# Optimization experiments

Hardware: AMD Instinct MI355X
Metric: run time of the kernel (lower is better)

## Reference

```python
import jax, jax.numpy as jnp
import numpy as np

N = 20000        # nodes
E = 1000000      # typed message-passing edges
R_REL = 32       # num relation types (== out_dim)
H = 128          # hidden_dim
IN = 128         # in_dim
B = 8            # num bases
ET = 20000       # target edges for decoder


def setup_inputs() -> dict:
    key = jax.random.key(0)
    ks = jax.random.split(key, 14)
    s = 0.05  # small init scale to keep relu/sigmoid in a sane range
    x = jax.random.normal(ks[0], (N, IN), jnp.float32)
    edge_index = jax.random.randint(ks[1], (2, E), 0, N, dtype=jnp.int64)
    etype = jax.random.randint(ks[2], (E,), 0, R_REL)
    edge_attr = jax.nn.one_hot(etype, R_REL, dtype=jnp.float32)  # one-hot so nonzero() == (arange(E), etype)
    target_edge_index = jax.random.randint(ks[3], (2, ET), 0, N, dtype=jnp.int64)
    return {
        'x': x,
        'edge_index': edge_index,
        'edge_attr': edge_attr,
        'target_edge_index': target_edge_index,
        'bases1': jax.random.normal(ks[4], (B, IN, H), jnp.float32) * s,
        'comp1': jax.random.normal(ks[5], (R_REL, B), jnp.float32) * s,
        'root1': jax.random.normal(ks[6], (IN, H), jnp.float32) * s,
        'bias1': jnp.zeros((H,), jnp.float32),
        'bases2': jax.random.normal(ks[7], (B, H, H), jnp.float32) * s,
        'comp2': jax.random.normal(ks[8], (R_REL, B), jnp.float32) * s,
        'root2': jax.random.normal(ks[9], (H, H), jnp.float32) * s,
        'bias2': jnp.zeros((H,), jnp.float32),
        'R_mat': jax.random.normal(ks[10], (H, H), jnp.float32) * s,
        'D': jax.random.normal(ks[11], (R_REL, H), jnp.float32) * s,
    }


def _rgcn(x, src, dst, etype, bases, comp, root, bias):
    # PyG-style RGCNConv with basis decomposition and per-relation mean aggregation.
    x_src = x[src]                                   # [E, in]  (memory-bound gather)
    seg = dst * R_REL + etype                        # segment per (dst node, relation)
    summ = jax.ops.segment_sum(x_src, seg, num_segments=N * R_REL)          # [N*R, in]
    cnt = jax.ops.segment_sum(jnp.ones((src.shape[0],), x.dtype), seg,
                              num_segments=N * R_REL)
    m = (summ / jnp.maximum(cnt, 1.0)[:, None]).reshape(N, R_REL, -1)       # per-relation mean
    W = jnp.einsum('rb,bio->rio', comp, bases)       # [R, in, out] relation weights from bases
    return jnp.einsum('nri,rio->no', m, W) + x @ root + bias


def reference(x, edge_index, edge_attr, target_edge_index,
              bases1, comp1, root1, bias1,
              bases2, comp2, root2, bias2,
              R_mat, D):
    # torch.nonzero(one-hot edge_attr) -> edges == arange(E), edge_type == argmax
    etype = jnp.argmax(edge_attr, axis=1)
    src, dst = edge_index[0], edge_index[1]
    h = jax.nn.relu(_rgcn(x, src, dst, etype, bases1, comp1, root1, bias1))   # dropout = identity (eval)
    h = jax.nn.relu(_rgcn(h, src, dst, etype, bases2, comp2, root2, bias2))
    x1 = h[target_edge_index[0]]                     # [ET, H]
    x2 = h[target_edge_index[1]]                     # [ET, H]
    # DEDICOM decoder: diag(D_r) @ R @ diag(D_r); equivalent to the diag-of-matmul-chain in the source
    M = D[:, :, None] * R_mat[None, :, :] * D[:, None, :]   # [R, H, H]
    out = jnp.einsum('ei,rij,ej->er', x1, M, x2)             # [ET, R]
    return jax.nn.sigmoid(out)
```

## Files before the change

kernel.cpp:

```cpp
#include <hip/hip_runtime.h>
#include <hip/hip_bf16.h>
#include <math.h>

#define NND 20000
#define NE  1000000
#define RREL 32
#define HD 128
#define NB 8
#define NT 20000
#define KCAT 1152
#define NBLK 64
#define CHUNK ((NE + NBLK - 1) / NBLK)

typedef short bf16x8 __attribute__((ext_vector_type(8)));
typedef float f32x4 __attribute__((ext_vector_type(4)));

static __device__ __forceinline__ unsigned short f2bf(float f){
  union { float f; unsigned int u; } c; c.f = f;
  unsigned int r = c.u + 0x7FFF + ((c.u >> 16) & 1);
  return (unsigned short)(r >> 16);
}
static __device__ __forceinline__ float bf2f(unsigned short s){
  union { unsigned int u; float f; } c; c.u = ((unsigned int)s) << 16;
  return c.f;
}

__global__ __launch_bounds__(256) void k_etype(
    const float* __restrict__ ea, int* __restrict__ etype)
{
  int e = blockIdx.x*256 + threadIdx.x;
  if (e >= NE) return;
  const float4* row = (const float4*)(ea + (size_t)e*RREL);
  int bi = 0;
  #pragma unroll
  for (int q=0;q<8;q++){
    float4 v = row[q];
    if (v.x > 0.5f) bi = q*4;
    if (v.y > 0.5f) bi = q*4+1;
    if (v.z > 0.5f) bi = q*4+2;
    if (v.w > 0.5f) bi = q*4+3;
  }
  etype[e] = bi;
}

__global__ __launch_bounds__(1024) void k_hist(const int* __restrict__ ei,
                                               int* __restrict__ ghist)
{
  __shared__ int h[NND/2];
  int t = threadIdx.x, b = blockIdx.x;
  for (int i=t; i<NND/2; i+=1024) h[i] = 0;
  __syncthreads();
  int e0 = b*CHUNK, e1 = min(e0+CHUNK, NE);
  for (int e=e0+t; e<e1; e+=1024){
    int dst = ei[NE + e];
    atomicAdd(&h[dst>>1], 1 << ((dst&1)*16));
  }
  __syncthreads();
  for (int i=t; i<NND/2; i+=1024){
    int v = h[i];
    ghist[(size_t)(2*i  )*NBLK + b] = v & 0xFFFF;
    ghist[(size_t)(2*i+1)*NBLK + b] = (v >> 16) & 0xFFFF;
  }
}

__global__ __launch_bounds__(256) void k_rowsum(const int* __restrict__ ghist,
                                                int* __restrict__ node_cnt)
{
  int t = threadIdx.x;
  int n = blockIdx.x*4 + (t>>6);
  int lane = t & 63;
  int v = ghist[(size_t)n*NBLK + lane];
  #pragma unroll
  for (int d=32; d>0; d>>=1) v += __shfl_down(v, d);
  if (lane == 0) node_cnt[n] = v;
}

__global__ __launch_bounds__(1024) void k_scan(const int* __restrict__ node_cnt,
                                               int* __restrict__ node_off)
{
  __shared__ int part[1024];
  int t = threadIdx.x;
  const int CH = (NND + 1023)/1024;
  int base = t*CH;
  int s = 0;
  for (int i=0;i<CH;i++){ int idx = base+i; if (idx<NND) s += node_cnt[idx]; }
  part[t] = s;
  __syncthreads();
  for (int d=1; d<1024; d<<=1){
    int v = part[t];
    int u = (t>=d) ? part[t-d] : 0;
    __syncthreads();
    part[t] = v + u;
    __syncthreads();
  }
  int run = (t==0) ? 0 : part[t-1];
  for (int i=0;i<CH;i++){ int idx=base+i; if (idx<NND){ node_off[idx]=run; run += node_cnt[idx]; } }
  if (t==1023) node_off[NND] = part[1023];
}

__global__ __launch_bounds__(256) void k_scanB(int* __restrict__ ghist,
                                               const int* __restrict__ node_off)
{
  int t = threadIdx.x;
  int n = blockIdx.x*4 + (t>>6);
  int lane = t & 63;
  int v = ghist[(size_t)n*NBLK + lane];
  int x = v;
  #pragma unroll
  for (int d=1; d<64; d<<=1){ int y = __shfl_up(x, d); if (lane >= d) x += y; }
  ghist[(size_t)n*NBLK + lane] = node_off[n] + x - v;
}

__global__ __launch_bounds__(1024) void k_scatter2(
    const int* __restrict__ ei, const int* __restrict__ etype,
    const int* __restrict__ ghist, int2* __restrict__ sorted)
{
  __shared__ int h[NND/2];
  int t = threadIdx.x, b = blockIdx.x;
  for (int i=t; i<NND/2; i+=1024) h[i] = 0;
  __syncthreads();
  int e0 = b*CHUNK, e1 = min(e0+CHUNK, NE);
  for (int e=e0+t; e<e1; e+=1024){
    int dst = ei[NE + e];
    int sh = (dst&1)*16;
    int old = atomicAdd(&h[dst>>1], 1 << sh);
    int rank = (old >> sh) & 0xFFFF;
    int pos = ghist[(size_t)dst*NBLK + b] + rank;
    sorted[pos] = make_int2(ei[e], etype[e]);
  }
}

__global__ __launch_bounds__(256) void k_cnt(const int2* __restrict__ sorted,
                                             const int* __restrict__ node_off,
                                             float* __restrict__ inv)
{
  int t = threadIdx.x;
  int n = blockIdx.x*4 + (t>>6);
  int lane = t & 63;
  int r = lane & 31, half = lane >> 5;
  int p0 = node_off[n], p1 = node_off[n+1];
  int c = 0;
  for (int p=p0+half; p<p1; p+=2) c += (sorted[p].y == r);
  c += __shfl_down(c, 32);
  if (lane < 32) inv[(size_t)n*RREL + lane] = 1.0f / fmaxf((float)c, 1.0f);
}

__global__ __launch_bounds__(256) void k_castX(const float* __restrict__ x,
                                               unsigned short* __restrict__ xb)
{
  int i = blockIdx.x*256 + threadIdx.x;
  if (i >= NND*HD/8) return;
  const float4* p = (const float4*)(x + (size_t)i*8);
  float4 a = p[0], b = p[1];
  unsigned int o0 = f2bf(a.x) | ((unsigned int)f2bf(a.y)<<16);
  unsigned int o1 = f2bf(a.z) | ((unsigned int)f2bf(a.w)<<16);
  unsigned int o2 = f2bf(b.x) | ((unsigned int)f2bf(b.y)<<16);
  unsigned int o3 = f2bf(b.z) | ((unsigned int)f2bf(b.w)<<16);
  *(uint4*)(xb + (size_t)i*8) = make_uint4(o0,o1,o2,o3);
}

__global__ __launch_bounds__(64) void k_agg(
    const int2* __restrict__ sorted, const int* __restrict__ node_off,
    const float* __restrict__ inv_cnt, const float* __restrict__ comp,
    const unsigned short* __restrict__ xb, unsigned short* __restrict__ mbxb)
{
  int n = blockIdx.x;
  int lane = threadIdx.x;
  float a0[NB], a1[NB];
  #pragma unroll
  for (int b=0;b<NB;b++){ a0[b]=0.f; a1[b]=0.f; }
  int p0 = node_off[n], p1 = node_off[n+1];
  const float* icr = inv_cnt + (size_t)n*RREL;
  for (int p=p0; p<p1; ++p){
    int2 se = sorted[p];
    float x0 = bf2f(xb[(size_t)se.x*HD + lane]);
    float x1 = bf2f(xb[(size_t)se.x*HD + 64 + lane]);
    float ic = icr[se.y];
    const float* cr = comp + se.y*NB;
    #pragma unroll
    for (int b=0;b<NB;b++){
      float c = cr[b]*ic;
      a0[b] += c*x0;
      a1[b] += c*x1;
    }
  }
  unsigned short* o = mbxb + (size_t)n*KCAT;
  #pragma unroll
  for (int b=0;b<NB;b++){
    o[b*HD + lane]      = f2bf(a0[b]);
    o[b*HD + 64 + lane] = f2bf(a1[b]);
  }
  o[1024 + lane]      = xb[(size_t)n*HD + lane];
  o[1024 + 64 + lane] = xb[(size_t)n*HD + 64 + lane];
}

__global__ __launch_bounds__(256) void k_prepW(
    const float* __restrict__ bases, const float* __restrict__ root,
    unsigned short* __restrict__ Wt)
{
  int idx = blockIdx.x*256 + threadIdx.x;
  if (idx >= HD*(KCAT/8)) return;
  int o  = idx / (KCAT/8);
  int k0 = (idx % (KCAT/8))*8;
  unsigned short tmp[8];
  #pragma unroll
  for (int q=0;q<8;q++){
    int k = k0+q;
    float v = (k < 1024) ? bases[(size_t)k*HD + o] : root[(size_t)(k-1024)*HD + o];
    tmp[q] = f2bf(v);
  }
  *(uint4*)(Wt + (size_t)o*KCAT + k0) = *(uint4*)tmp;
}

__global__ __launch_bounds__(256) void k_gemm2(
    const unsigned short* __restrict__ A, const unsigned short* __restrict__ Wt,
    const float* __restrict__ bias, float* __restrict__ outF,
    unsigned short* __restrict__ outB)
{
  int t = threadIdx.x, bm = blockIdx.x;
  int lane = t & 63, w = t >> 6, g = lane >> 4, c = lane & 15;
  const unsigned short* arow = A + (size_t)(bm*16 + c)*KCAT;
  const unsigned short* wt0 = Wt + (size_t)((w*2+0)*16 + c)*KCAT;
  const unsigned short* wt1 = Wt + (size_t)((w*2+1)*16 + c)*KCAT;
  f32x4 acc0 = {0.f,0.f,0.f,0.f}, acc1 = {0.f,0.f,0.f,0.f};
  for (int kk=0; kk<KCAT/32; ++kk){
    int koff = kk*32 + 8*g;
    bf16x8 a  = *(const bf16x8*)(arow + koff);
    bf16x8 b0 = *(const bf16x8*)(wt0 + koff);
    bf16x8 b1 = *(const bf16x8*)(wt1 + koff);
    acc0 = __builtin_amdgcn_mfma_f32_16x16x32_bf16(a, b0, acc0, 0,0,0);
    acc1 = __builtin_amdgcn_mfma_f32_16x16x32_bf16(a, b1, acc1, 0,0,0);
  }
  int orow = bm*16 + 4*g;
  #pragma unroll
  for (int nt=0; nt<2; ++nt){
    int o = (w*2+nt)*16 + c;
    float bi = bias[o];
    f32x4 acc = nt ? acc1 : acc0;
    #pragma unroll
    for (int q=0; q<4; ++q){
      int rr = orow + q;
      float v = fmaxf(acc[q] + bi, 0.f);
      outF[(size_t)rr*HD + o] = v;
      outB[(size_t)rr*HD + o] = f2bf(v);
    }
  }
}

__global__ __launch_bounds__(256) void k_prep(const float* __restrict__ Rm,
                                              const float* __restrict__ D,
                                              unsigned short* __restrict__ Ms)
{
  int r = blockIdx.x, t = threadIdx.x;
  int i = blockIdx.y*16 + (t>>4);
  int j0 = (t&15)*8;
  float di = D[r*HD + i];
  float4 dj0 = *(const float4*)(D + r*HD + j0);
  float4 dj1 = *(const float4*)(D + r*HD + j0 + 4);
  float4 r0 = *(const float4*)(Rm + (size_t)i*HD + j0);
  float4 r1 = *(const float4*)(Rm + (size_t)i*HD + j0 + 4);
  unsigned int o0 = f2bf(di*dj0.x*r0.x) | ((unsigned int)f2bf(di*dj0.y*r0.y)<<16);
  unsigned int o1 = f2bf(di*dj0.z*r0.z) | ((unsigned int)f2bf(di*dj0.w*r0.w)<<16);
  unsigned int o2 = f2bf(di*dj1.x*r1.x) | ((unsigned int)f2bf(di*dj1.y*r1.y)<<16);
  unsigned int o3 = f2bf(di*dj1.z*r1.z) | ((unsigned int)f2bf(di*dj1.w*r1.w)<<16);
  *(uint4*)(Ms + (size_t)(r*HD + i)*HD + j0) = make_uint4(o0,o1,o2,o3);
}

__global__ __launch_bounds__(256) void k_dec3(
    const float* __restrict__ h2, const int* __restrict__ tgt,
    const unsigned short* __restrict__ Ms, float* __restrict__ out)
{
  __shared__ __align__(16) unsigned short vb[64*136];
  __shared__ __align__(16) float uf[64*132];
  __shared__ __align__(16) float red[64*8];
  int t = threadIdx.x;
  int bm = blockIdx.x;
  int lane = t & 63, w = t >> 6, g = lane >> 4, c = lane & 15;

  {
    int e = t >> 2, seg = t & 3;
    int eg = bm*64 + e;
    bool ok = (eg < NT);
    int n0 = ok ? tgt[eg] : 0;
    int n1 = ok ? tgt[NT + eg] : 0;
    const float4* pu = (const float4*)(h2 + (size_t)n0*HD + seg*32);
    const float4* pv = (const float4*)(h2 + (size_t)n1*HD + seg*32);
    float* ufr = uf + e*132 + seg*32;
    unsigned int* vbr = (unsigned int*)vb + e*68 + seg*16;
    #pragma unroll
    for (int q=0;q<8;q++){
      float4 u4 = ok ? pu[q] : make_float4(0,0,0,0);
      float4 v4 = ok ? pv[q] : make_float4(0,0,0,0);
      *(float4*)(ufr + q*4) = u4;
      vbr[q*2+0] = (unsigned int)f2bf(v4.x) | ((unsigned int)f2bf(v4.y)<<16);
      vbr[q*2+1] = (unsigned int)f2bf(v4.z) | ((unsigned int)f2bf(v4.w)<<16);
    }
  }
  __syncthreads();

  for (int r=0; r<RREL; ++r){
    f32x4 acc[2][4];
    #pragma unroll
    for (int mm=0;mm<2;mm++)
      #pragma unroll
      for (int nt=0;nt<4;nt++){ f32x4 z = {0.f,0.f,0.f,0.f}; acc[mm][nt] = z; }
    #pragma unroll
    for (int kk=0; kk<4; ++kk){
      int koff = kk*32 + 8*g;
      bf16x8 a0 = *(const bf16x8*)(Ms + (size_t)(r*HD + (2*w+0)*16 + c)*HD + koff);
      bf16x8 a1 = *(const bf16x8*)(Ms + (size_t)(r*HD + (2*w+1)*16 + c)*HD + koff);
      #pragma unroll
      for (int nt=0; nt<4; ++nt){
        bf16x8 b = *(const bf16x8*)&vb[(nt*16 + c)*136 + koff];
        acc[0][nt] = __builtin_amdgcn_mfma_f32_16x16x32_bf16(a0, b, acc[0][nt], 0,0,0);
        acc[1][nt] = __builtin_amdgcn_mfma_f32_16x16x32_bf16(a1, b, acc[1][nt], 0,0,0);
      }
    }
    float s[4];
    #pragma unroll
    for (int nt=0; nt<4; ++nt){
      int e = nt*16 + c;
      float4 u0 = *(const float4*)&uf[e*132 + (2*w+0)*16 + 4*g];
      float4 u1 = *(const float4*)&uf[e*132 + (2*w+1)*16 + 4*g];
      s[nt] = u0.x*acc[0][nt][0] + u0.y*acc[0][nt][1] + u0.z*acc[0][nt][2] + u0.w*acc[0][nt][3]
            + u1.x*acc[1][nt][0] + u1.y*acc[1][nt][1] + u1.z*acc[1][nt][2] + u1.w*acc[1][nt][3];
      s[nt] += __shfl_xor(s[nt], 16);
      s[nt] += __shfl_xor(s[nt], 32);
    }
    if (lane < 16){
      #pragma unroll
      for (int nt=0; nt<4; ++nt) red[(nt*16 + lane)*8 + w] = s[nt];
    }
    __syncthreads();
    if (t < 64){
      float4 v4 = *(const float4*)&red[t*8];
      float sum = v4.x + v4.y + v4.z + v4.w;
      int eg = bm*64 + t;
      if (eg < NT) out[(size_t)eg*RREL + r] = 1.f/(1.f+expf(-sum));
    }
    __syncthreads();
  }
}

extern "C" void kernel_launch(void* const* d_in, const int* in_sizes, int n_in,
                              void* d_out, int out_size, void* d_ws, size_t ws_size,
                              hipStream_t stream)
{
  const float* x      = (const float*)d_in[0];
  const int*   ei     = (const int*)d_in[1];
  const float* ea     = (const float*)d_in[2];
  const int*   tgt    = (const int*)d_in[3];
  const float* bases1 = (const float*)d_in[4];
  const float* comp1  = (const float*)d_in[5];
  const float* root1  = (const float*)d_in[6];
  const float* bias1  = (const float*)d_in[7];
  const float* bases2 = (const float*)d_in[8];
  const float* comp2  = (const float*)d_in[9];
  const float* root2  = (const float*)d_in[10];
  const float* bias2  = (const float*)d_in[11];
  const float* Rm     = (const float*)d_in[12];
  const float* D      = (const float*)d_in[13];
  float* out = (float*)d_out;

  char* base = (char*)d_ws;
  size_t o = 0;
  auto carve = [&](size_t bytes)->char*{
    char* p = base + o;
    o += (bytes + 255) & ~(size_t)255;
    return p;
  };
  int*   etype     = (int*)  carve((size_t)NE*4);
  int*   ghist     = (int*)  carve((size_t)NND*NBLK*4);
  float* inv_cnt   = (float*)carve((size_t)NND*RREL*4);
  int*   node_cnt  = (int*)  carve((size_t)NND*4);
  int*   node_off  = (int*)  carve((size_t)(NND+1)*4);
  int2*  sorted    = (int2*) carve((size_t)NE*8);
  unsigned short* mbxb = (unsigned short*)carve((size_t)NND*KCAT*2);
  float* h1        = (float*)carve((size_t)NND*HD*4);
  float* h2        = (float*)carve((size_t)NND*HD*4);
  unsigned short* xb  = (unsigned short*)carve((size_t)NND*HD*2);
  unsigned short* h1b = (unsigned short*)carve((size_t)NND*HD*2);
  unsigned short* h2b = (unsigned short*)carve((size_t)NND*HD*2);
  unsigned short* Ms  = (unsigned short*)carve((size_t)RREL*HD*HD*2);
  unsigned short* Wt1 = (unsigned short*)carve((size_t)HD*KCAT*2);
  unsigned short* Wt2 = (unsigned short*)carve((size_t)HD*KCAT*2);

  if (ws_size < o) return;

  k_etype   <<<(NE+255)/256, 256, 0, stream>>>(ea, etype);
  k_hist    <<<NBLK, 1024, 0, stream>>>(ei, ghist);
  k_rowsum  <<<NND/4, 256, 0, stream>>>(ghist, node_cnt);
  k_scan    <<<1, 1024, 0, stream>>>(node_cnt, node_off);
  k_scanB   <<<NND/4, 256, 0, stream>>>(ghist, node_off);
  k_scatter2<<<NBLK, 1024, 0, stream>>>(ei, etype, ghist, sorted);
  k_cnt     <<<NND/4, 256, 0, stream>>>(sorted, node_off, inv_cnt);

  k_castX<<<(NND*HD/8+255)/256, 256, 0, stream>>>(x, xb);
  k_prepW<<<(HD*(KCAT/8)+255)/256, 256, 0, stream>>>(bases1, root1, Wt1);
  k_prepW<<<(HD*(KCAT/8)+255)/256, 256, 0, stream>>>(bases2, root2, Wt2);
  k_prep <<<dim3(RREL, 8), 256, 0, stream>>>(Rm, D, Ms);

  k_agg  <<<NND, 64, 0, stream>>>(sorted, node_off, inv_cnt, comp1, xb, mbxb);
  k_gemm2<<<NND/16, 256, 0, stream>>>(mbxb, Wt1, bias1, h1, h1b);
  k_agg  <<<NND, 64, 0, stream>>>(sorted, node_off, inv_cnt, comp2, h1b, mbxb);
  k_gemm2<<<NND/16, 256, 0, stream>>>(mbxb, Wt2, bias2, h2, h2b);

  k_dec3<<<(NT+63)/64, 256, 0, stream>>>(h2, tgt, Ms, out);
}
```

Measured before the change: 520.0 us.

## Vectorize aggregation loads and split decoder relations across a 2D grid

In k_agg, each lane now loads two adjacent bf16 values as one 32-bit word and writes packed pairs, which halves the load/store instruction count in the per-edge gather loop. The decoder kernel gets a second grid dimension that splits the 32 relations into 4 groups of 8, raising the block count so more of the GPU is busy. It also reads the v operand from the existing bf16 copy of h2 instead of converting fp32 on the fly, and keeps the u operand in registers rather than shared memory. The cost is that each node's target rows are gathered four times across blocks, and the per-lane column mapping in aggregation changes.

New measurement: 499.2 us. 1.04x faster.

```diff
diff --git a/kernel.cpp b/kernel.cpp
--- a/kernel.cpp
+++ b/kernel.cpp
@@ -173,10 +173,11 @@
   const float* icr = inv_cnt + (size_t)n*RREL;
   for (int p=p0; p<p1; ++p){
     int2 se = sorted[p];
-    float x0 = bf2f(xb[(size_t)se.x*HD + lane]);
-    float x1 = bf2f(xb[(size_t)se.x*HD + 64 + lane]);
+    unsigned int vv = *(const unsigned int*)(xb + (size_t)se.x*HD + 2*lane);
     float ic = icr[se.y];
     const float* cr = comp + se.y*NB;
+    float x0 = bf2f((unsigned short)(vv & 0xFFFF));
+    float x1 = bf2f((unsigned short)(vv >> 16));
     #pragma unroll
     for (int b=0;b<NB;b++){
       float c = cr[b]*ic;
@@ -187,11 +188,10 @@
   unsigned short* o = mbxb + (size_t)n*KCAT;
   #pragma unroll
   for (int b=0;b<NB;b++){
-    o[b*HD + lane]      = f2bf(a0[b]);
-    o[b*HD + 64 + lane] = f2bf(a1[b]);
-  }
-  o[1024 + lane]      = xb[(size_t)n*HD + lane];
-  o[1024 + 64 + lane] = xb[(size_t)n*HD + 64 + lane];
+    unsigned int u = (unsigned int)f2bf(a0[b]) | ((unsigned int)f2bf(a1[b])<<16);
+    *(unsigned int*)(o + b*HD + 2*lane) = u;
+  }
+  *(unsigned int*)(o + 1024 + 2*lane) = *(const unsigned int*)(xb + (size_t)n*HD + 2*lane);
 }
 
 __global__ __launch_bounds__(256) void k_prepW(
@@ -267,12 +267,12 @@
 }
 
 __global__ __launch_bounds__(256) void k_dec3(
-    const float* __restrict__ h2, const int* __restrict__ tgt,
+    const float* __restrict__ h2, const unsigned short* __restrict__ h2b,
+    const int* __restrict__ tgt,
     const unsigned short* __restrict__ Ms, float* __restrict__ out)
 {
   __shared__ __align__(16) unsigned short vb[64*136];
-  __shared__ __align__(16) float uf[64*132];
-  __shared__ __align__(16) float red[64*8];
+  __shared__ __align__(16) float red[4][72];
   int t = threadIdx.x;
   int bm = blockIdx.x;
   int lane = t & 63, w = t >> 6, g = lane >> 4, c = lane & 15;
@@ -281,24 +281,30 @@
     int e = t >> 2, seg = t & 3;
     int eg = bm*64 + e;
     bool ok = (eg < NT);
+    int n1 = ok ? tgt[NT + eg] : 0;
+    const uint4* pv = (const uint4*)(h2b + (size_t)n1*HD);
+    unsigned int* vbr = (unsigned int*)vb + e*68;
+    #pragma unroll
+    for (int q=0; q<4; ++q){
+      uint4 v4 = ok ? pv[seg*4+q] : make_uint4(0,0,0,0);
+      *(uint4*)(vbr + (seg*4+q)*4) = v4;
+    }
+  }
+  float4 ur[4][2];
+  #pragma unroll
+  for (int nt=0; nt<4; ++nt){
+    int eg = bm*64 + nt*16 + c;
+    bool ok = (eg < NT);
     int n0 = ok ? tgt[eg] : 0;
-    int n1 = ok ? tgt[NT + eg] : 0;
-    const float4* pu = (const float4*)(h2 + (size_t)n0*HD + seg*32);
-    const float4* pv = (const float4*)(h2 + (size_t)n1*HD + seg*32);
-    float* ufr = uf + e*132 + seg*32;
-    unsigned int* vbr = (unsigned int*)vb + e*68 + seg*16;
-    #pragma unroll
-    for (int q=0;q<8;q++){
-      float4 u4 = ok ? pu[q] : make_float4(0,0,0,0);
-      float4 v4 = ok ? pv[q] : make_float4(0,0,0,0);
-      *(float4*)(ufr + q*4) = u4;
-      vbr[q*2+0] = (unsigned int)f2bf(v4.x) | ((unsigned int)f2bf(v4.y)<<16);
-      vbr[q*2+1] = (unsigned int)f2bf(v4.z) | ((unsigned int)f2bf(v4.w)<<16);
-    }
+    const float* pu = h2 + (size_t)n0*HD;
+    float4 z = make_float4(0,0,0,0);
+    ur[nt][0] = ok ? *(const float4*)(pu + (2*w+0)*16 + 4*g) : z;
+    ur[nt][1] = ok ? *(const float4*)(pu + (2*w+1)*16 + 4*g) : z;
   }
   __syncthreads();
 
-  for (int r=0; r<RREL; ++r){
+  for (int rr=0; rr<8; ++rr){
+    int r = blockIdx.y*8 + rr;
     f32x4 acc[2][4];
     #pragma unroll
     for (int mm=0;mm<2;mm++)
@@ -319,22 +325,20 @@
     float s[4];
     #pragma unroll
     for (int nt=0; nt<4; ++nt){
-      int e = nt*16 + c;
-      float4 u0 = *(const float4*)&uf[e*132 + (2*w+0)*16 + 4*g];
-      float4 u1 = *(const float4*)&uf[e*132 + (2*w+1)*16 + 4*g];
-      s[nt] = u0.x*acc[0][nt][0] + u0.y*acc[0][nt][1] + u0.z*acc[0][nt][2] + u0.w*acc[0][nt][3]
-            + u1.x*acc[1][nt][0] + u1.y*acc[1][nt][1] + u1.z*acc[1][nt][2] + u1.w*acc[1][nt][3];
+      s[nt] = ur[nt][0].x*acc[0][nt][0] + ur[nt][0].y*acc[0][nt][1]
+            + ur[nt][0].z*acc[0][nt][2] + ur[nt][0].w*acc[0][nt][3]
+            + ur[nt][1].x*acc[1][nt][0] + ur[nt][1].y*acc[1][nt][1]
+            + ur[nt][1].z*acc[1][nt][2] + ur[nt][1].w*acc[1][nt][3];
       s[nt] += __shfl_xor(s[nt], 16);
       s[nt] += __shfl_xor(s[nt], 32);
     }
     if (lane < 16){
       #pragma unroll
-      for (int nt=0; nt<4; ++nt) red[(nt*16 + lane)*8 + w] = s[nt];
+      for (int nt=0; nt<4; ++nt) red[w][nt*16 + lane] = s[nt];
     }
     __syncthreads();
     if (t < 64){
-      float4 v4 = *(const float4*)&red[t*8];
-      float sum = v4.x + v4.y + v4.z + v4.w;
+      float sum = red[0][t] + red[1][t] + red[2][t] + red[3][t];
       int eg = bm*64 + t;
       if (eg < NT) out[(size_t)eg*RREL + r] = 1.f/(1.f+expf(-sum));
     }
@@ -405,5 +409,6 @@
   k_agg  <<<NND, 64, 0, stream>>>(sorted, node_off, inv_cnt, comp2, h1b, mbxb);
   k_gemm2<<<NND/16, 256, 0, stream>>>(mbxb, Wt2, bias2, h2, h2b);
 
-  k_dec3<<<(NT+63)/64, 256, 0, stream>>>(h2, tgt, Ms, out);
-}
+  dim3 dgD((NT+63)/64, 4);
+  k_dec3<<<dgD, 256, 0, stream>>>(h2, h2b, tgt, Ms, out);
+}
```
